# Kernel optimization log

Measured on AMD Instinct MI355X. Metric: run time of the kernel, lower is better.

The kernel has to match this reference:

```python
import jax, jax.numpy as jnp
import numpy as np

NIN, NHID, NDECHID, NOUT = 128, 256, 512, 10
B, N = 32, 4096


def _linear_params(key, fan_in, fan_out):
    kw, kb = jax.random.split(key)
    bound = 1.0 / np.sqrt(fan_in)
    W = jax.random.uniform(kw, (fan_in, fan_out), jnp.float32, -bound, bound)
    b = jax.random.uniform(kb, (fan_out,), jnp.float32, -bound, bound)
    return W, b


def setup_inputs() -> dict:
    key = jax.random.key(0)
    ks = jax.random.split(key, 7)
    x = jax.random.normal(ks[0], (B, N, NIN), jnp.float32)
    W1, b1 = _linear_params(ks[1], NIN, NHID)
    W2, b2 = _linear_params(ks[2], NHID, NHID)
    W3, b3 = _linear_params(ks[3], NHID, NHID)
    D1, c1 = _linear_params(ks[4], NHID, NDECHID)
    D2, c2 = _linear_params(ks[5], NDECHID, NDECHID)
    D3, c3 = _linear_params(ks[6], NDECHID, NOUT)
    return {"x": x, "W1": W1, "b1": b1, "W2": W2, "b2": b2, "W3": W3, "b3": b3,
            "D1": D1, "c1": c1, "D2": D2, "c2": c2, "D3": D3, "c3": c3}


def reference(x, W1, b1, W2, b2, W3, b3, D1, c1, D2, c2, D3, c3):
    # encoder MLP: Linear-ReLU-Linear-ReLU-Linear, then extra ReLU
    h = jax.nn.relu(x @ W1 + b1)            # [B, N, nhid]
    h = jax.nn.relu(h @ W2 + b2)
    h = jax.nn.relu(h @ W3 + b3)            # fused enc output + F.relu
    # mean_{i,j}(h_i * h_j) over the set == (mean_i h)^2 elementwise (exact identity)
    m = jnp.mean(h, axis=1)                  # [B, nhid]
    p = jax.nn.relu(m * m)                   # [B, nhid]
    # decoder MLP
    d = jax.nn.relu(p @ D1 + c1)
    d = jax.nn.relu(d @ D2 + c2)
    return d @ D3 + c3                       # [B, nout]
```

## Files before the change

kernel.cpp:

```cpp
#include <hip/hip_runtime.h>
#include <hip/hip_bf16.h>
#include <stdint.h>


#define NIN   128
#define NHID  256
#define NDEC  512
#define NOUTC 10
#define BATCH 32
#define NTOK  4096
#define MTILE 64
#define NBLK  (BATCH * (NTOK / MTILE))

#define SW2(t) (((t) & 15) << 4)

typedef short bf16x8 __attribute__((ext_vector_type(8)));
typedef float floatx4 __attribute__((ext_vector_type(4)));
typedef long  longx2  __attribute__((ext_vector_type(2)));

__device__ __forceinline__ uint16_t f2b(float f) {
  union { uint32_t u; float f; } v; v.f = f;
  uint32_t r = v.u + 0x7FFFu + ((v.u >> 16) & 1u);
  return (uint16_t)(r >> 16);
}
__device__ __forceinline__ uint32_t pkbf(float lo, float hi) {
  __hip_bfloat162 h = __float22bfloat162_rn(float2{lo, hi});
  union { __hip_bfloat162 h; uint32_t u; } c; c.h = h;
  return c.u;
}

__global__ __launch_bounds__(256) void pack_weights(
    const float* __restrict__ W1, const float* __restrict__ W2,
    const float* __restrict__ W3, const float* __restrict__ c3,
    uint8_t* __restrict__ pW, float* __restrict__ msum,
    float* __restrict__ out) {
  int p = blockIdx.x * blockDim.x + threadIdx.x;
  if (p < BATCH * NHID) msum[p] = 0.f;
  if (p < BATCH * NOUTC) out[p] = c3[p % NOUTC];
  if (p < 32768) {
    int j = p & 7, ln = (p >> 3) & 63, rest = p >> 9;
    int kc = rest & 3, mt = rest >> 2;
    int m = mt * 16 + (ln & 15);
    int k = kc * 32 + ((ln >> 4) << 3) + j;
    ((uint16_t*)pW)[p] = f2b(W1[k * NHID + m]);
  } else {
    int p2 = p - 32768;
    const float* W = (p2 < 65536) ? W2 : W3;
    int base = (p2 < 65536) ? 65536 : 131072;
    if (p2 >= 65536) p2 -= 65536;
    int j = p2 & 7, ln = (p2 >> 3) & 63, rest = p2 >> 9;
    int kc = rest & 7, mt = rest >> 3;
    int m = mt * 16 + (ln & 15);
    int k = kc * 32 + ((ln >> 4) << 3) + j;
    int r = __builtin_amdgcn_cvt_pk_fp8_f32(W[k * NHID + m], 0.f, 0, false);
    pW[base + p2] = (uint8_t)(r & 0xFF);
  }
}

__global__ __launch_bounds__(512) void encoder(
    const float* __restrict__ x,
    const uint8_t* __restrict__ pW,
    const float* __restrict__ b1,
    const float* __restrict__ b2,
    const float* __restrict__ b3,
    float* __restrict__ msum) {
  __shared__ __align__(16) uint8_t Hs0[MTILE * 256];
  __shared__ __align__(16) uint8_t Hs1[MTILE * 256];
  __shared__ __align__(16) float scr[NHID];

  const int tid  = threadIdx.x;
  const int wave = tid >> 6;
  const int lane = tid & 63;
  const int l15  = lane & 15;
  const int q    = lane >> 4;
  const int tok0  = blockIdx.x * MTILE;
  const int batch = blockIdx.x >> 6;

  const uint16_t* pW1 = (const uint16_t*)pW;
  const uint8_t*  pW2 = pW + 65536;
  const uint8_t*  pW3 = pW + 131072;

  {
    const float4* xv = (const float4*)(x + (size_t)tok0 * NIN);
#pragma unroll
    for (int i = 0; i < 2; ++i) {
      const int u = tid + i * 512;
      float4 va = xv[2 * u];
      float4 vb = xv[2 * u + 1];
      uint4 w = make_uint4(pkbf(va.x, va.y), pkbf(va.z, va.w),
                           pkbf(vb.x, vb.y), pkbf(vb.z, vb.w));
      const int row = u >> 4;
      const int cb  = (u & 15) << 4;
      *(uint4*)&Hs0[row * 256 + (cb ^ SW2(row))] = w;
    }
  }
  __syncthreads();

  floatx4 acc[2][4];

#pragma unroll
  for (int jt = 0; jt < 2; ++jt) {
    const float4 bb = *(const float4*)&b1[(wave * 2 + jt) * 16 + q * 4];
#pragma unroll
    for (int tt = 0; tt < 4; ++tt)
      acc[jt][tt] = (floatx4){bb.x, bb.y, bb.z, bb.w};
  }
#pragma unroll
  for (int kc = 0; kc < 4; ++kc) {
    bf16x8 a0 = *(const bf16x8*)(pW1 + ((((wave * 2 + 0) * 4 + kc) * 64 + lane) << 3));
    bf16x8 a1 = *(const bf16x8*)(pW1 + ((((wave * 2 + 1) * 4 + kc) * 64 + lane) << 3));
#pragma unroll
    for (int tt = 0; tt < 4; ++tt) {
      const int t = tt * 16 + l15;
      bf16x8 b = *(const bf16x8*)&Hs0[t * 256 + ((kc * 64 + q * 16) ^ SW2(t))];
      acc[0][tt] = __builtin_amdgcn_mfma_f32_16x16x32_bf16(a0, b, acc[0][tt], 0, 0, 0);
      acc[1][tt] = __builtin_amdgcn_mfma_f32_16x16x32_bf16(a1, b, acc[1][tt], 0, 0, 0);
    }
  }
#pragma unroll
  for (int jt = 0; jt < 2; ++jt) {
    const int j0 = (wave * 2 + jt) * 16 + q * 4;
    const int pb = ((j0 >> 3) & 3) * 64 + (j0 >> 5) * 8 + (j0 & 7);
#pragma unroll
    for (int tt = 0; tt < 4; ++tt) {
      const int t = tt * 16 + l15;
      float v0 = fmaxf(acc[jt][tt][0], 0.f);
      float v1 = fmaxf(acc[jt][tt][1], 0.f);
      float v2 = fmaxf(acc[jt][tt][2], 0.f);
      float v3 = fmaxf(acc[jt][tt][3], 0.f);
      int u = __builtin_amdgcn_cvt_pk_fp8_f32(v0, v1, 0, false);
      u = __builtin_amdgcn_cvt_pk_fp8_f32(v2, v3, u, true);
      *(uint32_t*)&Hs1[t * 256 + (pb ^ SW2(t))] = (uint32_t)u;
    }
  }
  __syncthreads();

#pragma unroll
  for (int jt = 0; jt < 2; ++jt) {
    const float4 bb = *(const float4*)&b2[(wave * 2 + jt) * 16 + q * 4];
#pragma unroll
    for (int tt = 0; tt < 4; ++tt)
      acc[jt][tt] = (floatx4){bb.x, bb.y, bb.z, bb.w};
  }
#pragma unroll
  for (int kc2 = 0; kc2 < 4; ++kc2) {
    longx2 b[4];
#pragma unroll
    for (int tt = 0; tt < 4; ++tt) {
      const int t = tt * 16 + l15;
      b[tt] = *(const longx2*)&Hs1[t * 256 + ((q * 64 + kc2 * 16) ^ SW2(t))];
    }
#pragma unroll
    for (int s = 0; s < 2; ++s) {
      const int kc = kc2 * 2 + s;
      long a0 = *(const long*)(pW2 + ((((wave * 2 + 0) * 8 + kc) * 64 + lane) << 3));
      long a1 = *(const long*)(pW2 + ((((wave * 2 + 1) * 8 + kc) * 64 + lane) << 3));
#pragma unroll
      for (int tt = 0; tt < 4; ++tt) {
        acc[0][tt] = __builtin_amdgcn_mfma_f32_16x16x32_fp8_fp8(a0, b[tt][s], acc[0][tt], 0, 0, 0);
        acc[1][tt] = __builtin_amdgcn_mfma_f32_16x16x32_fp8_fp8(a1, b[tt][s], acc[1][tt], 0, 0, 0);
      }
    }
  }
#pragma unroll
  for (int jt = 0; jt < 2; ++jt) {
    const int j0 = (wave * 2 + jt) * 16 + q * 4;
    const int pb = ((j0 >> 3) & 3) * 64 + (j0 >> 5) * 8 + (j0 & 7);
#pragma unroll
    for (int tt = 0; tt < 4; ++tt) {
      const int t = tt * 16 + l15;
      float v0 = fmaxf(acc[jt][tt][0], 0.f);
      float v1 = fmaxf(acc[jt][tt][1], 0.f);
      float v2 = fmaxf(acc[jt][tt][2], 0.f);
      float v3 = fmaxf(acc[jt][tt][3], 0.f);
      int u = __builtin_amdgcn_cvt_pk_fp8_f32(v0, v1, 0, false);
      u = __builtin_amdgcn_cvt_pk_fp8_f32(v2, v3, u, true);
      *(uint32_t*)&Hs0[t * 256 + (pb ^ SW2(t))] = (uint32_t)u;
    }
  }
  __syncthreads();

#pragma unroll
  for (int jt = 0; jt < 2; ++jt) {
    const float4 bb = *(const float4*)&b3[(wave * 2 + jt) * 16 + q * 4];
#pragma unroll
    for (int tt = 0; tt < 4; ++tt)
      acc[jt][tt] = (floatx4){bb.x, bb.y, bb.z, bb.w};
  }
#pragma unroll
  for (int kc2 = 0; kc2 < 4; ++kc2) {
    longx2 b[4];
#pragma unroll
    for (int tt = 0; tt < 4; ++tt) {
      const int t = tt * 16 + l15;
      b[tt] = *(const longx2*)&Hs0[t * 256 + ((q * 64 + kc2 * 16) ^ SW2(t))];
    }
#pragma unroll
    for (int s = 0; s < 2; ++s) {
      const int kc = kc2 * 2 + s;
      long a0 = *(const long*)(pW3 + ((((wave * 2 + 0) * 8 + kc) * 64 + lane) << 3));
      long a1 = *(const long*)(pW3 + ((((wave * 2 + 1) * 8 + kc) * 64 + lane) << 3));
#pragma unroll
      for (int tt = 0; tt < 4; ++tt) {
        acc[0][tt] = __builtin_amdgcn_mfma_f32_16x16x32_fp8_fp8(a0, b[tt][s], acc[0][tt], 0, 0, 0);
        acc[1][tt] = __builtin_amdgcn_mfma_f32_16x16x32_fp8_fp8(a1, b[tt][s], acc[1][tt], 0, 0, 0);
      }
    }
  }

#pragma unroll
  for (int jt = 0; jt < 2; ++jt) {
    float s0 = 0.f, s1 = 0.f, s2 = 0.f, s3 = 0.f;
#pragma unroll
    for (int tt = 0; tt < 4; ++tt) {
      s0 += fmaxf(acc[jt][tt][0], 0.f);
      s1 += fmaxf(acc[jt][tt][1], 0.f);
      s2 += fmaxf(acc[jt][tt][2], 0.f);
      s3 += fmaxf(acc[jt][tt][3], 0.f);
    }
#pragma unroll
    for (int m = 1; m <= 8; m <<= 1) {
      s0 += __shfl_xor(s0, m);
      s1 += __shfl_xor(s1, m);
      s2 += __shfl_xor(s2, m);
      s3 += __shfl_xor(s3, m);
    }
    if (l15 == 0)
      *(float4*)&scr[(wave * 2 + jt) * 16 + q * 4] = (float4){s0, s1, s2, s3};
  }
  __syncthreads();
  if (tid < NHID)
    atomicAdd(&msum[batch * NHID + tid], scr[tid]);
}

__global__ __launch_bounds__(1024) void decoder(
    const float* __restrict__ msum,
    const float* __restrict__ D1, const float* __restrict__ c1,
    const float* __restrict__ D2, const float* __restrict__ c2,
    const float* __restrict__ D3,
    float* __restrict__ out) {
  __shared__ float p[NHID];
  __shared__ float d1[NDEC];
  __shared__ float d2q[128];
  __shared__ __align__(16) float red[4096];
  const int b = blockIdx.x >> 2, qd = blockIdx.x & 3, t = threadIdx.x;

  if (t < NHID) {
    float m = msum[b * NHID + t] * (1.f / NTOK);
    p[t] = m * m;
  }
  __syncthreads();

  {
    const int jg = t & 127;
    const int ks = t >> 7;
    const float4* D1v = (const float4*)D1;
    float4 s = {0.f, 0.f, 0.f, 0.f};
    for (int k = ks * 32; k < ks * 32 + 32; ++k) {
      float4 w = D1v[k * 128 + jg];
      float pv = p[k];
      s.x += pv * w.x; s.y += pv * w.y; s.z += pv * w.z; s.w += pv * w.w;
    }
    *(float4*)&red[t * 4] = s;
    __syncthreads();
    if (t < NDEC) {
      float v = c1[t];
#pragma unroll
      for (int i = 0; i < 8; ++i) v += red[i * 512 + t];
      d1[t] = fmaxf(v, 0.f);
    }
    __syncthreads();
  }

  {
    const int jg2 = t & 31;
    const int ks2 = t >> 5;
    const float4* D2v = (const float4*)D2;
    float4 s = {0.f, 0.f, 0.f, 0.f};
    for (int k = ks2 * 16; k < ks2 * 16 + 16; ++k) {
      float4 w = D2v[k * 128 + qd * 32 + jg2];
      float hv = d1[k];
      s.x += hv * w.x; s.y += hv * w.y; s.z += hv * w.z; s.w += hv * w.w;
    }
    *(float4*)&red[t * 4] = s;
    __syncthreads();
    if (t < 128) {
      float v = c2[qd * 128 + t];
#pragma unroll
      for (int i = 0; i < 32; ++i) v += red[i * 128 + t];
      d2q[t] = fmaxf(v, 0.f);
    }
    __syncthreads();
  }

  {
    const int j3 = t & 15;
    const int kc = t >> 4;
    float s = 0.f;
    if (j3 < NOUTC)
      for (int k = kc * 2; k < kc * 2 + 2; ++k)
        s += d2q[k] * D3[(qd * 128 + k) * NOUTC + j3];
    red[t] = s;
    __syncthreads();
    if (t < NOUTC) {
      float v = 0.f;
#pragma unroll
      for (int i = 0; i < 64; ++i) v += red[i * 16 + t];
      atomicAdd(&out[b * NOUTC + t], v);
    }
  }
}

extern "C" void kernel_launch(void* const* d_in, const int* in_sizes, int n_in,
                              void* d_out, int out_size, void* d_ws, size_t ws_size,
                              hipStream_t stream) {
  const float* x  = (const float*)d_in[0];
  const float* W1 = (const float*)d_in[1];
  const float* b1 = (const float*)d_in[2];
  const float* W2 = (const float*)d_in[3];
  const float* b2 = (const float*)d_in[4];
  const float* W3 = (const float*)d_in[5];
  const float* b3 = (const float*)d_in[6];
  const float* D1 = (const float*)d_in[7];
  const float* c1 = (const float*)d_in[8];
  const float* D2 = (const float*)d_in[9];
  const float* c2 = (const float*)d_in[10];
  const float* D3 = (const float*)d_in[11];
  const float* c3 = (const float*)d_in[12];

  uint8_t* pW   = (uint8_t*)d_ws;
  float*   msum = (float*)((char*)d_ws + 384 * 1024);

  pack_weights<<<640, 256, 0, stream>>>(W1, W2, W3, c3, pW, msum,
                                        (float*)d_out);
  encoder<<<NBLK, 512, 0, stream>>>(x, pW, b1, b2, b3, msum);
  decoder<<<128, 1024, 0, stream>>>(msum, D1, c1, D2, c2, D3,
                                    (float*)d_out);
}
```

Before: 155.1 us.

## Repack fp8 weights for 16-byte loads and reduce via LDS instead of shuffles

The prepack kernel now stores the W2/W3 fp8 fragments so each lane's 64 K-bytes for one m-tile are contiguous. The encoder can then fetch two K-chunks with a single 16-byte load per kc2, where it previously issued two 8-byte loads. The final column reduction drops the 16-lane xor-shuffle tree: lanes write partial float4 sums to a padded LDS scratch that reuses the Hs1 region, and 256 threads each sum 16 entries before the atomic. This trims global load instructions and cross-lane shuffles, at the cost of more LDS traffic and a serial 16-element sum per thread.

After: 153.9 us. About the same (-0.8%).

```diff
diff --git a/kernel.cpp b/kernel.cpp
--- a/kernel.cpp
+++ b/kernel.cpp
@@ -53,7 +53,7 @@
     int m = mt * 16 + (ln & 15);
     int k = kc * 32 + ((ln >> 4) << 3) + j;
     int r = __builtin_amdgcn_cvt_pk_fp8_f32(W[k * NHID + m], 0.f, 0, false);
-    pW[base + p2] = (uint8_t)(r & 0xFF);
+    pW[base + (mt * 64 + ln) * 64 + kc * 8 + j] = (uint8_t)(r & 0xFF);
   }
 }
 
@@ -64,9 +64,9 @@
     const float* __restrict__ b2,
     const float* __restrict__ b3,
     float* __restrict__ msum) {
-  __shared__ __align__(16) uint8_t Hs0[MTILE * 256];
-  __shared__ __align__(16) uint8_t Hs1[MTILE * 256];
-  __shared__ __align__(16) float scr[NHID];
+  __shared__ __align__(16) uint8_t HsAll[33792];
+  uint8_t* Hs0 = HsAll;
+  uint8_t* Hs1 = HsAll + 16384;
 
   const int tid  = threadIdx.x;
   const int wave = tid >> 6;
@@ -144,6 +144,8 @@
   }
 #pragma unroll
   for (int kc2 = 0; kc2 < 4; ++kc2) {
+    longx2 a0 = *(const longx2*)(pW2 + ((wave * 2 + 0) * 64 + lane) * 64 + kc2 * 16);
+    longx2 a1 = *(const longx2*)(pW2 + ((wave * 2 + 1) * 64 + lane) * 64 + kc2 * 16);
     longx2 b[4];
 #pragma unroll
     for (int tt = 0; tt < 4; ++tt) {
@@ -152,13 +154,10 @@
     }
 #pragma unroll
     for (int s = 0; s < 2; ++s) {
-      const int kc = kc2 * 2 + s;
-      long a0 = *(const long*)(pW2 + ((((wave * 2 + 0) * 8 + kc) * 64 + lane) << 3));
-      long a1 = *(const long*)(pW2 + ((((wave * 2 + 1) * 8 + kc) * 64 + lane) << 3));
 #pragma unroll
       for (int tt = 0; tt < 4; ++tt) {
-        acc[0][tt] = __builtin_amdgcn_mfma_f32_16x16x32_fp8_fp8(a0, b[tt][s], acc[0][tt], 0, 0, 0);
-        acc[1][tt] = __builtin_amdgcn_mfma_f32_16x16x32_fp8_fp8(a1, b[tt][s], acc[1][tt], 0, 0, 0);
+        acc[0][tt] = __builtin_amdgcn_mfma_f32_16x16x32_fp8_fp8(a0[s], b[tt][s], acc[0][tt], 0, 0, 0);
+        acc[1][tt] = __builtin_amdgcn_mfma_f32_16x16x32_fp8_fp8(a1[s], b[tt][s], acc[1][tt], 0, 0, 0);
       }
     }
   }
@@ -189,6 +188,8 @@
   }
 #pragma unroll
   for (int kc2 = 0; kc2 < 4; ++kc2) {
+    longx2 a0 = *(const longx2*)(pW3 + ((wave * 2 + 0) * 64 + lane) * 64 + kc2 * 16);
+    longx2 a1 = *(const longx2*)(pW3 + ((wave * 2 + 1) * 64 + lane) * 64 + kc2 * 16);
     longx2 b[4];
 #pragma unroll
     for (int tt = 0; tt < 4; ++tt) {
@@ -197,40 +198,40 @@
     }
 #pragma unroll
     for (int s = 0; s < 2; ++s) {
-      const int kc = kc2 * 2 + s;
-      long a0 = *(const long*)(pW3 + ((((wave * 2 + 0) * 8 + kc) * 64 + lane) << 3));
-      long a1 = *(const long*)(pW3 + ((((wave * 2 + 1) * 8 + kc) * 64 + lane) << 3));
 #pragma unroll
       for (int tt = 0; tt < 4; ++tt) {
-        acc[0][tt] = __builtin_amdgcn_mfma_f32_16x16x32_fp8_fp8(a0, b[tt][s], acc[0][tt], 0, 0, 0);
-        acc[1][tt] = __builtin_amdgcn_mfma_f32_16x16x32_fp8_fp8(a1, b[tt][s], acc[1][tt], 0, 0, 0);
+        acc[0][tt] = __builtin_amdgcn_mfma_f32_16x16x32_fp8_fp8(a0[s], b[tt][s], acc[0][tt], 0, 0, 0);
+        acc[1][tt] = __builtin_amdgcn_mfma_f32_16x16x32_fp8_fp8(a1[s], b[tt][s], acc[1][tt], 0, 0, 0);
       }
     }
   }
 
-#pragma unroll
-  for (int jt = 0; jt < 2; ++jt) {
-    float s0 = 0.f, s1 = 0.f, s2 = 0.f, s3 = 0.f;
-#pragma unroll
-    for (int tt = 0; tt < 4; ++tt) {
-      s0 += fmaxf(acc[jt][tt][0], 0.f);
-      s1 += fmaxf(acc[jt][tt][1], 0.f);
-      s2 += fmaxf(acc[jt][tt][2], 0.f);
-      s3 += fmaxf(acc[jt][tt][3], 0.f);
-    }
-#pragma unroll
-    for (int m = 1; m <= 8; m <<= 1) {
-      s0 += __shfl_xor(s0, m);
-      s1 += __shfl_xor(s1, m);
-      s2 += __shfl_xor(s2, m);
-      s3 += __shfl_xor(s3, m);
-    }
-    if (l15 == 0)
-      *(float4*)&scr[(wave * 2 + jt) * 16 + q * 4] = (float4){s0, s1, s2, s3};
-  }
-  __syncthreads();
-  if (tid < NHID)
-    atomicAdd(&msum[batch * NHID + tid], scr[tid]);
+  {
+    float4* scratch = (float4*)(HsAll + 16384);
+#pragma unroll
+    for (int jt = 0; jt < 2; ++jt) {
+      float s0 = 0.f, s1 = 0.f, s2 = 0.f, s3 = 0.f;
+#pragma unroll
+      for (int tt = 0; tt < 4; ++tt) {
+        s0 += fmaxf(acc[jt][tt][0], 0.f);
+        s1 += fmaxf(acc[jt][tt][1], 0.f);
+        s2 += fmaxf(acc[jt][tt][2], 0.f);
+        s3 += fmaxf(acc[jt][tt][3], 0.f);
+      }
+      scratch[((wave * 2 + jt) * 4 + q) * 17 + l15] = (float4){s0, s1, s2, s3};
+    }
+  }
+  __syncthreads();
+  if (tid < NHID) {
+    const float* sf = (const float*)(HsAll + 16384);
+    const int row = ((tid >> 4) << 2) + ((tid >> 2) & 3);
+    const int r = tid & 3;
+    float v = 0.f;
+#pragma unroll
+    for (int l = 0; l < 16; ++l)
+      v += sf[row * 68 + l * 4 + r];
+    atomicAdd(&msum[batch * NHID + tid], v);
+  }
 }
 
 __global__ __launch_bounds__(1024) void decoder(
```
